# Performance work log

Measured on AMD Instinct MI355X. Metric: run time of the kernel, lower is better.

The kernel has to match this reference:

```python
import jax, jax.numpy as jnp
import numpy as np

G, NPG = 2048, 512          # glimpses, points per glimpse
N0 = G * NPG                # 1,048,576 input points
CPG, CPG2 = 128, 32         # clusters per glimpse at level1/level2
M1, M2 = G * CPG, G * CPG2  # 262144, 65536


def _seg_mean_np(x, ids, m):
    cnt = np.bincount(ids, minlength=m).astype(np.float32)
    out = np.stack([np.bincount(ids, weights=x[:, d], minlength=m) for d in range(x.shape[1])], axis=1)
    return (out / np.maximum(cnt, 1.0)[:, None]).astype(np.float32)


def setup_inputs() -> dict:
    key = jax.random.key(0)
    ks = jax.random.split(key, 16)
    rng = np.random.default_rng(0)
    pos_np = (rng.random((N0, 3)) * 4.0).astype(np.float32)
    # voxel_mean_pool level 0: each point -> a cluster within its glimpse
    g_of_pt = np.arange(N0) // NPG
    out_index0 = (g_of_pt * CPG + rng.integers(0, CPG, N0)).astype(np.int64)
    pos1_np = _seg_mean_np(pos_np, out_index0, M1)
    g_of_c1 = np.arange(M1) // CPG
    out_index1 = (g_of_c1 * CPG2 + rng.integers(0, CPG2, M1)).astype(np.int64)
    pos2_np = _seg_mean_np(pos1_np, out_index1, M2)
    out_index2 = (np.arange(M2) // CPG2).astype(np.int64)  # glimpse id per level-2 point

    def w(k, shp, s=0.05):
        return jax.random.normal(k, shp, dtype=jnp.float32) * s

    return {
        "rgb": jax.random.normal(ks[0], (N0, 1), dtype=jnp.float32),
        "pos": jnp.asarray(pos_np), "pos1": jnp.asarray(pos1_np), "pos2": jnp.asarray(pos2_np),
        "out_index0": jnp.asarray(out_index0), "out_index1": jnp.asarray(out_index1),
        "out_index2": jnp.asarray(out_index2),
        "eps": jax.random.normal(ks[1], (G, 128), dtype=jnp.float32),
        # conv1: local (c_in=1 + 3 -> 16), global (16 -> 32)
        "W1l": w(ks[2], (4, 16)), "b1l": jnp.zeros(16), "W1g": w(ks[3], (16, 32)), "b1g": jnp.zeros(32),
        # conv2: (32+3 -> 64), (64 -> 128)
        "W2l": w(ks[4], (35, 64)), "b2l": jnp.zeros(64), "W2g": w(ks[5], (64, 128)), "b2g": jnp.zeros(128),
        # conv3: (128+3 -> 128), (128 -> 256)
        "W3l": w(ks[6], (131, 128)), "b3l": jnp.zeros(128), "W3g": w(ks[7], (128, 256)), "b3g": jnp.zeros(256),
        "Wlin": w(ks[8], (256, 256)), "blin": jnp.zeros(256),
    }


def _point_conv(x_in, pos_in, pos_out, out_index, Wl, bl, Wg, bg):
    # gather relative position of each input point w.r.t. its output center
    rel = pos_in - pos_out[out_index]                      # [E,3]
    h = jax.nn.celu(jnp.concatenate([x_in, rel], -1) @ Wl + bl)  # per-edge MLP
    m = pos_out.shape[0]
    cnt = jax.ops.segment_sum(jnp.ones((h.shape[0],), h.dtype), out_index, num_segments=m)
    agg = jax.ops.segment_sum(h, out_index, num_segments=m) / jnp.maximum(cnt, 1.0)[:, None]
    return agg @ Wg + bg


def reference(rgb, pos, pos1, pos2, out_index0, out_index1, out_index2, eps,
              W1l, b1l, W1g, b1g, W2l, b2l, W2g, b2g, W3l, b3l, W3g, b3g, Wlin, blin):
    f = rgb  # ar=False path: feature = rgb
    f = jax.nn.celu(_point_conv(f, pos, pos1, out_index0, W1l, b1l, W1g, b1g))   # [M1,32]
    f = jax.nn.celu(_point_conv(f, pos1, pos2, out_index1, W2l, b2l, W2g, b2g))  # [M2,128]
    centers = jnp.zeros((G, 3), f.dtype)  # pos_sample = zeros_like(glimpse__center)
    f = jax.nn.celu(_point_conv(f, pos2, centers, out_index2, W3l, b3l, W3g, b3g))  # [G,256]
    out = f @ Wlin + blin
    mu, sg = jnp.split(out, 2, axis=1)
    sigma = jax.nn.softplus(sg)  # to_sigma
    z = mu + sigma * eps         # Normal.rsample
    z_what, z_mask = jnp.split(z, 2, axis=1)
    return z_what, z_mask, mu, sigma, f
```

## Files before the change

### kernel.cpp

```cpp
#include <hip/hip_runtime.h>
#include <hip/hip_bf16.h>
#include <cstddef>

#define G_   2048
#define NPG_ 512
#define CPG_ 128
#define CPG2_ 32

#define OFF_ZW 0
#define OFF_ZM (G_*64)
#define OFF_MU (2*G_*64)
#define OFF_SG (2*G_*64 + G_*128)
#define OFF_F  (2*G_*64 + 2*G_*128)

typedef __attribute__((ext_vector_type(8))) short bf16x8;
typedef __attribute__((ext_vector_type(4))) float f32x4;

__device__ __forceinline__ float celu_f(float x)     { return x > 0.f ? x : __expf(x) - 1.f; }
__device__ __forceinline__ float softplus_f(float x) { return fmaxf(x, 0.f) + __logf(1.f + __expf(-fabsf(x))); }
__device__ __forceinline__ unsigned short f2bf(float x) {
    unsigned u = __float_as_uint(x);
    u += 0x7FFFu + ((u >> 16) & 1u);
    return (unsigned short)(u >> 16);
}
__device__ __forceinline__ unsigned pack2(float a, float b) {
    unsigned ua = __float_as_uint(a); ua += 0x7FFFu + ((ua >> 16) & 1u);
    unsigned ub = __float_as_uint(b); ub += 0x7FFFu + ((ub >> 16) & 1u);
    return (ua >> 16) | (ub & 0xFFFF0000u);
}
__device__ __forceinline__ float bflo(unsigned w) { return __uint_as_float(w << 16); }
__device__ __forceinline__ float bfhi(unsigned w) { return __uint_as_float(w & 0xffff0000u); }
__device__ __forceinline__ bf16x8 ldb8(const unsigned short* p) {
    union { uint2 u[2]; bf16x8 v; } x;
    x.u[0] = *(const uint2*)p;
    x.u[1] = *(const uint2*)(p + 4);
    return x.v;
}

__global__ void k_prep(const float* __restrict__ W2l, const float* __restrict__ W2g,
                       const float* __restrict__ W3l, const float* __restrict__ W3g,
                       const float* __restrict__ Wlin, const float* __restrict__ W1g,
                       unsigned short* __restrict__ w2lT, unsigned short* __restrict__ w2gT,
                       unsigned short* __restrict__ w3lT, unsigned short* __restrict__ w3gT,
                       unsigned short* __restrict__ wlinT, unsigned short* __restrict__ w1gT)
{
    const int tid = blockIdx.x*256 + threadIdx.x, stride = gridDim.x*256;
    for (int i = tid; i < 64*64; i += stride) {
        const int ch = i >> 6, k = i & 63;
        w2lT[i] = f2bf(k < 35 ? W2l[k*64 + ch] : 0.f);
    }
    for (int i = tid; i < 128*64; i += stride) {
        const int ch = i >> 6, k = i & 63;
        w2gT[i] = f2bf(W2g[k*128 + ch]);
    }
    for (int i = tid; i < 128*160; i += stride) {
        const int ch = i / 160, k = i % 160;
        w3lT[i] = f2bf(k < 131 ? W3l[k*128 + ch] : 0.f);
    }
    for (int i = tid; i < 256*128; i += stride) {
        const int ch = i >> 7, k = i & 127;
        w3gT[i] = f2bf(W3g[k*256 + ch]);
    }
    for (int i = tid; i < 256*256; i += stride) {
        const int ch = i >> 8, k = i & 255;
        wlinT[i] = f2bf(Wlin[k*256 + ch]);
    }
    for (int i = tid; i < 32*40; i += stride) {
        const int ch = i / 40, k = i % 40;
        w1gT[i] = f2bf(k < 16 ? W1g[k*32 + ch] : 0.f);
    }
}

__global__ __launch_bounds__(256, 6) void k_fused(
    const float* __restrict__ rgb, const float* __restrict__ pos, const float* __restrict__ pos1,
    const float* __restrict__ pos2, const int* __restrict__ idx0, const int* __restrict__ idx1,
    const float* __restrict__ W1l, const float* __restrict__ b1l,
    const unsigned short* __restrict__ w1gT, const float* __restrict__ b1g,
    const unsigned short* __restrict__ w2lT, const float* __restrict__ b2l,
    const unsigned short* __restrict__ w2gT, const float* __restrict__ b2g,
    const unsigned short* __restrict__ w3lT, const float* __restrict__ b3l,
    unsigned short* __restrict__ aggws)
{
    const int g = blockIdx.x, t = threadIdx.x;
    const int lane = t & 63, wv = t >> 6;
    const int lr = lane & 15, quad = lane >> 4;

    __shared__ __align__(16) unsigned char smem[27008];
    uint2* const spts = (uint2*)smem;
    unsigned short* const aggT = (unsigned short*)(smem + 4096);
    unsigned short* const xs16 = (unsigned short*)smem;
    unsigned short* const HT   = (unsigned short*)smem;
    unsigned short* const xs3  = (unsigned short*)smem;
    int* const cnt   = (int*)(smem + 18432);
    int* const start = (int*)(smem + 18944);
    int* const ctr   = (int*)(smem + 19456);
    int* const cnti  = (int*)(smem + 19968);
    unsigned short* const sT   = (unsigned short*)(smem + 18432);
    unsigned short* const agg2 = (unsigned short*)(smem + 18432);
    float* const red  = (float*)(smem + 18432);
    float* const invc = (float*)(smem + 26880);

    if (t < CPG_) cnt[t] = 0;
    if (t < CPG2_) cnti[t] = 0;
    int slc_r = 0;
    float relx = 0.f, rely = 0.f, relz = 0.f;
    if (t < CPG_) {
        const int c2 = idx1[g*CPG_ + t];
        slc_r = c2 - g*CPG2_;
        relx = pos1[(g*CPG_ + t)*3 + 0] - pos2[c2*3 + 0];
        rely = pos1[(g*CPG_ + t)*3 + 1] - pos2[c2*3 + 1];
        relz = pos1[(g*CPG_ + t)*3 + 2] - pos2[c2*3 + 2];
    }
    for (int i = t; i < 128*8; i += 256) {
        const int r = i >> 3, j = i & 7;
        ((unsigned*)aggT)[r*20 + 8 + j] = 0u;
    }
    __syncthreads();

    float px0[2], prx[2], pry[2], prz[2];
    int plc[2];
    #pragma unroll
    for (int r = 0; r < 2; r++) {
        const int lp = r*256 + t;
        const int p  = g*NPG_ + lp;
        const int c  = idx0[p];
        plc[r] = c - g*CPG_;
        px0[r] = rgb[p];
        prx[r] = pos[p*3+0] - pos1[c*3+0];
        pry[r] = pos[p*3+1] - pos1[c*3+1];
        prz[r] = pos[p*3+2] - pos1[c*3+2];
        atomicAdd(&cnt[plc[r]], 1);
    }
    if (t < CPG_) atomicAdd(&cnti[slc_r], 1);
    __syncthreads();

    if (t < CPG_) {
        int val = cnt[t];
        const int ln = t & 63;
        #pragma unroll
        for (int d = 1; d < 64; d <<= 1) {
            const int v = __shfl_up(val, d, 64);
            if (ln >= d) val += v;
        }
        ctr[t] = val;
    }
    __syncthreads();
    if (t < CPG_) {
        int v = ctr[t];
        if (t >= 64) v += ctr[63];
        const int s = v - cnt[t];
        start[t] = s; ctr[t] = s;
    }
    if (t < CPG2_) invc[t] = 1.f / fmaxf((float)cnti[t], 1.f);
    __syncthreads();

    #pragma unroll
    for (int r = 0; r < 2; r++) {
        const int slot = atomicAdd(&ctr[plc[r]], 1);
        uint2 pk;
        pk.x = pack2(px0[r], prx[r]);
        pk.y = pack2(pry[r], prz[r]);
        spts[slot] = pk;
    }
    __syncthreads();

    {
        const int c = t >> 1, ch0 = (t & 1) * 8;
        float wj[8], wx[8], wy[8], wz[8], bb2[8];
        #pragma unroll
        for (int j = 0; j < 8; j++) {
            wj[j] = W1l[ch0+j]; wx[j] = W1l[16+ch0+j];
            wy[j] = W1l[32+ch0+j]; wz[j] = W1l[48+ch0+j];
            bb2[j] = b1l[ch0+j];
        }
        float a[8];
        #pragma unroll
        for (int j = 0; j < 8; j++) a[j] = 0.f;
        const int n = cnt[c], base = start[c];
        for (int i = 0; i < n; i++) {
            const uint2 pk = spts[base + i];
            const float x0 = bflo(pk.x), rx = bfhi(pk.x);
            const float ry = bflo(pk.y), rz = bfhi(pk.y);
            #pragma unroll
            for (int j = 0; j < 8; j++) {
                const float h = bb2[j] + x0*wj[j] + rx*wx[j] + ry*wy[j] + rz*wz[j];
                a[j] += celu_f(h);
            }
        }
        const float inv = 1.f / fmaxf((float)n, 1.f);
        uint2 q0, q1;
        q0.x = pack2(a[0]*inv, a[1]*inv);
        q0.y = pack2(a[2]*inv, a[3]*inv);
        q1.x = pack2(a[4]*inv, a[5]*inv);
        q1.y = pack2(a[6]*inv, a[7]*inv);
        *(uint2*)&aggT[c*40 + ch0]     = q0;
        *(uint2*)&aggT[c*40 + ch0 + 4] = q1;
    }
    __syncthreads();

    f32x4 c1[2][2];
    {
        #pragma unroll
        for (int nt = 0; nt < 2; nt++) {
            const float bias = b1g[nt*16 + lr];
            c1[nt][0] = (f32x4){bias, bias, bias, bias};
            c1[nt][1] = (f32x4){bias, bias, bias, bias};
        }
        const bf16x8 b0 = *(const bf16x8*)&w1gT[(0*16 + lr)*40 + quad*8];
        const bf16x8 b1 = *(const bf16x8*)&w1gT[(1*16 + lr)*40 + quad*8];
        #pragma unroll
        for (int mt = 0; mt < 2; mt++) {
            const bf16x8 a = *(const bf16x8*)&aggT[((2*wv + mt)*16 + lr)*40 + quad*8];
            c1[0][mt] = __builtin_amdgcn_mfma_f32_16x16x32_bf16(a, b0, c1[0][mt], 0, 0, 0);
            c1[1][mt] = __builtin_amdgcn_mfma_f32_16x16x32_bf16(a, b1, c1[1][mt], 0, 0, 0);
        }
    }
    __syncthreads();

    {
        const uint4 z4 = {0u, 0u, 0u, 0u};
        for (int i = t; i < 528; i += 256) ((uint4*)sT)[i] = z4;
    }
    #pragma unroll
    for (int nt = 0; nt < 2; nt++)
    #pragma unroll
    for (int mt = 0; mt < 2; mt++)
    #pragma unroll
    for (int r = 0; r < 4; r++) {
        const int cl = (2*wv + mt)*16 + quad*4 + r;
        xs16[cl*72 + nt*16 + lr] = f2bf(celu_f(c1[nt][mt][r]));
    }
    if (t < CPG_) {
        xs16[t*72 + 32] = f2bf(relx);
        xs16[t*72 + 33] = f2bf(rely);
        xs16[t*72 + 34] = f2bf(relz);
    }
    for (int i = t; i < 128*29; i += 256) {
        const int r = i / 29, c = 35 + (i - r*29);
        xs16[r*72 + c] = 0;
    }
    __syncthreads();

    if (t < CPG_) sT[slc_r*132 + t] = 0x3F80;
    float hv[8][4];
    {
        const int chn = wv*16 + lr;
        const bf16x8 bw0 = *(const bf16x8*)&w2lT[chn*64 + quad*8];
        const bf16x8 bw1 = *(const bf16x8*)&w2lT[chn*64 + 32 + quad*8];
        const float bias = b2l[chn];
        #pragma unroll
        for (int m = 0; m < 8; m++) {
            f32x4 acc = (f32x4){bias, bias, bias, bias};
            const bf16x8 a0 = *(const bf16x8*)&xs16[(m*16 + lr)*72 + quad*8];
            const bf16x8 a1 = *(const bf16x8*)&xs16[(m*16 + lr)*72 + 32 + quad*8];
            acc = __builtin_amdgcn_mfma_f32_16x16x32_bf16(a0, bw0, acc, 0, 0, 0);
            acc = __builtin_amdgcn_mfma_f32_16x16x32_bf16(a1, bw1, acc, 0, 0, 0);
            #pragma unroll
            for (int r = 0; r < 4; r++) hv[m][r] = celu_f(acc[r]);
        }
    }
    __syncthreads();

    {
        const int chn = wv*16 + lr;
        #pragma unroll
        for (int m = 0; m < 8; m++) {
            uint2 p;
            p.x = pack2(hv[m][0], hv[m][1]);
            p.y = pack2(hv[m][2], hv[m][3]);
            *(uint2*)&HT[chn*136 + m*16 + quad*4] = p;
        }
    }
    __syncthreads();

    float aggv[2][4];
    {
        const int ch = wv*16 + lr;
        f32x4 acc[2];
        acc[0] = (f32x4){0.f, 0.f, 0.f, 0.f};
        acc[1] = (f32x4){0.f, 0.f, 0.f, 0.f};
        #pragma unroll
        for (int ks = 0; ks < 4; ks++) {
            const bf16x8 b = *(const bf16x8*)&HT[ch*136 + ks*32 + quad*8];
            #pragma unroll
            for (int mt = 0; mt < 2; mt++) {
                const bf16x8 a = ldb8(&sT[(mt*16 + lr)*132 + ks*32 + quad*8]);
                acc[mt] = __builtin_amdgcn_mfma_f32_16x16x32_bf16(a, b, acc[mt], 0, 0, 0);
            }
        }
        #pragma unroll
        for (int mt = 0; mt < 2; mt++)
        #pragma unroll
        for (int r = 0; r < 4; r++)
            aggv[mt][r] = acc[mt][r] * invc[mt*16 + quad*4 + r];
    }
    __syncthreads();

    {
        const int ch = wv*16 + lr;
        #pragma unroll
        for (int mt = 0; mt < 2; mt++)
        #pragma unroll
        for (int r = 0; r < 4; r++)
            agg2[(mt*16 + quad*4 + r)*72 + ch] = f2bf(aggv[mt][r]);
    }
    if (t < CPG2_) {
        #pragma unroll
        for (int d = 0; d < 3; d++)
            xs3[t*168 + 128 + d] = f2bf(pos2[(g*CPG2_ + t)*3 + d]);
    }
    for (int i = t; i < 32*29; i += 256) {
        const int r = i / 29, c = 131 + (i - r*29);
        xs3[r*168 + c] = 0;
    }
    __syncthreads();

    {
        f32x4 acc2[2][2];
        int   chn2[2];
        bf16x8 bw[2][2];
        #pragma unroll
        for (int nt = 0; nt < 2; nt++) {
            chn2[nt] = (wv + nt*4)*16 + lr;
            const float bias = b2g[chn2[nt]];
            #pragma unroll
            for (int mt = 0; mt < 2; mt++) acc2[nt][mt] = (f32x4){bias, bias, bias, bias};
            bw[nt][0] = *(const bf16x8*)&w2gT[chn2[nt]*64 + quad*8];
            bw[nt][1] = *(const bf16x8*)&w2gT[chn2[nt]*64 + 32 + quad*8];
        }
        #pragma unroll
        for (int ks = 0; ks < 2; ks++) {
            #pragma unroll
            for (int mt = 0; mt < 2; mt++) {
                const bf16x8 a = *(const bf16x8*)&agg2[(mt*16 + lr)*72 + ks*32 + quad*8];
                acc2[0][mt] = __builtin_amdgcn_mfma_f32_16x16x32_bf16(a, bw[0][ks], acc2[0][mt], 0, 0, 0);
                acc2[1][mt] = __builtin_amdgcn_mfma_f32_16x16x32_bf16(a, bw[1][ks], acc2[1][mt], 0, 0, 0);
            }
        }
        #pragma unroll
        for (int nt = 0; nt < 2; nt++)
        #pragma unroll
        for (int mt = 0; mt < 2; mt++)
        #pragma unroll
        for (int r = 0; r < 4; r++) {
            const int row = mt*16 + quad*4 + r;
            xs3[row*168 + chn2[nt]] = f2bf(celu_f(acc2[nt][mt][r]));
        }
    }
    __syncthreads();

    {
        f32x4 acc[2][2];
        int chn[2];
        #pragma unroll
        for (int nt = 0; nt < 2; nt++) {
            chn[nt] = (wv + nt*4)*16 + lr;
            const float bias = b3l[chn[nt]];
            #pragma unroll
            for (int mt = 0; mt < 2; mt++) acc[nt][mt] = (f32x4){bias, bias, bias, bias};
        }
        #pragma unroll
        for (int ks = 0; ks < 5; ks++) {
            const bf16x8 b0 = *(const bf16x8*)&w3lT[chn[0]*160 + ks*32 + quad*8];
            const bf16x8 b1 = *(const bf16x8*)&w3lT[chn[1]*160 + ks*32 + quad*8];
            #pragma unroll
            for (int mt = 0; mt < 2; mt++) {
                const bf16x8 a = *(const bf16x8*)&xs3[(mt*16 + lr)*168 + ks*32 + quad*8];
                acc[0][mt] = __builtin_amdgcn_mfma_f32_16x16x32_bf16(a, b0, acc[0][mt], 0, 0, 0);
                acc[1][mt] = __builtin_amdgcn_mfma_f32_16x16x32_bf16(a, b1, acc[1][mt], 0, 0, 0);
            }
        }
        #pragma unroll
        for (int nt = 0; nt < 2; nt++)
        #pragma unroll
        for (int mt = 0; mt < 2; mt++) {
            const float p = celu_f(acc[nt][mt][0]) + celu_f(acc[nt][mt][1])
                          + celu_f(acc[nt][mt][2]) + celu_f(acc[nt][mt][3]);
            red[chn[nt]*9 + mt*4 + quad] = p;
        }
    }
    __syncthreads();

    if (t < 128) {
        const float* rp = &red[t*9];
        float a = 0.f;
        #pragma unroll
        for (int p = 0; p < 8; p++) a += rp[p];
        aggws[(size_t)g*128 + t] = f2bf(a * (1.f/32.f));
    }
}

__global__ __launch_bounds__(256) void k_head(
    const unsigned short* __restrict__ aggws,
    const unsigned short* __restrict__ w3gT, const float* __restrict__ b3g,
    const unsigned short* __restrict__ wlinT, const float* __restrict__ blin,
    const float* __restrict__ eps, float* __restrict__ out)
{
    const int g0 = blockIdx.x * 16, t = threadIdx.x;
    const int lane = t & 63, wv = t >> 6;
    const int lr = lane & 15, quad = lane >> 4;
    __shared__ __align__(16) unsigned short aggB[16*136];
    __shared__ __align__(16) unsigned short f3B[16*264];

    {
        const int row = t >> 4, col8 = (t & 15) * 8;
        const uint4 v = ((const uint4*)aggws)[(size_t)g0*16 + t];
        *(uint4*)&aggB[row*136 + col8] = v;
    }
    __syncthreads();

    {
        f32x4 c3[4];
        int ch3[4];
        #pragma unroll
        for (int nt = 0; nt < 4; nt++) {
            ch3[nt] = (wv + nt*4)*16 + lr;
            const float bias = b3g[ch3[nt]];
            c3[nt] = (f32x4){bias, bias, bias, bias};
        }
        #pragma unroll
        for (int ks = 0; ks < 4; ks++) {
            const bf16x8 a = *(const bf16x8*)&aggB[lr*136 + ks*32 + quad*8];
            #pragma unroll
            for (int nt = 0; nt < 4; nt++) {
                const bf16x8 b = *(const bf16x8*)&w3gT[ch3[nt]*128 + ks*32 + quad*8];
                c3[nt] = __builtin_amdgcn_mfma_f32_16x16x32_bf16(a, b, c3[nt], 0, 0, 0);
            }
        }
        #pragma unroll
        for (int nt = 0; nt < 4; nt++)
        #pragma unroll
        for (int r = 0; r < 4; r++) {
            const int row = quad*4 + r;
            const float v = celu_f(c3[nt][r]);
            out[OFF_F + (size_t)(g0 + row)*256 + ch3[nt]] = v;
            f3B[row*264 + ch3[nt]] = f2bf(v);
        }
    }
    __syncthreads();

    {
        f32x4 cl[4];
        int ch4[4];
        #pragma unroll
        for (int nt = 0; nt < 4; nt++) {
            ch4[nt] = (wv + nt*4)*16 + lr;
            const float bias = blin[ch4[nt]];
            cl[nt] = (f32x4){bias, bias, bias, bias};
        }
        #pragma unroll
        for (int ks = 0; ks < 8; ks++) {
            const bf16x8 a = *(const bf16x8*)&f3B[lr*264 + ks*32 + quad*8];
            #pragma unroll
            for (int nt = 0; nt < 4; nt++) {
                const bf16x8 b = *(const bf16x8*)&wlinT[ch4[nt]*256 + ks*32 + quad*8];
                cl[nt] = __builtin_amdgcn_mfma_f32_16x16x32_bf16(a, b, cl[nt], 0, 0, 0);
            }
        }
        #pragma unroll
        for (int nt = 0; nt < 2; nt++)
        #pragma unroll
        for (int r = 0; r < 4; r++) {
            const int row = quad*4 + r;
            const int g = g0 + row;
            const int ch = ch4[nt];
            const float mu    = cl[nt][r];
            const float sigma = softplus_f(cl[nt + 2][r]);
            const float z     = mu + sigma * eps[(size_t)g*128 + ch];
            out[OFF_MU + (size_t)g*128 + ch] = mu;
            out[OFF_SG + (size_t)g*128 + ch] = sigma;
            if (nt == 0) out[OFF_ZW + (size_t)g*64 + ch] = z;
            else         out[OFF_ZM + (size_t)g*64 + (ch - 64)] = z;
        }
    }
}

extern "C" void kernel_launch(void* const* d_in, const int* in_sizes, int n_in,
                              void* d_out, int out_size, void* d_ws, size_t ws_size,
                              hipStream_t stream)
{
    const float* rgb  = (const float*)d_in[0];
    const float* pos  = (const float*)d_in[1];
    const float* pos1 = (const float*)d_in[2];
    const float* pos2 = (const float*)d_in[3];
    const int*   idx0 = (const int*)d_in[4];
    const int*   idx1 = (const int*)d_in[5];
    const float* eps  = (const float*)d_in[7];
    const float* W1l = (const float*)d_in[8],  *b1l = (const float*)d_in[9];
    const float* W1g = (const float*)d_in[10], *b1g = (const float*)d_in[11];
    const float* W2l = (const float*)d_in[12], *b2l = (const float*)d_in[13];
    const float* W2g = (const float*)d_in[14], *b2g = (const float*)d_in[15];
    const float* W3l = (const float*)d_in[16], *b3l = (const float*)d_in[17];
    const float* W3g = (const float*)d_in[18], *b3g = (const float*)d_in[19];
    const float* Wlin = (const float*)d_in[20], *blin = (const float*)d_in[21];

    unsigned short* w2lT  = (unsigned short*)d_ws;
    unsigned short* w2gT  = w2lT + 64*64;
    unsigned short* w3lT  = w2gT + 128*64;
    unsigned short* w3gT  = w3lT + 128*160;
    unsigned short* wlinT = w3gT + 256*128;
    unsigned short* w1gT  = wlinT + 256*256;
    unsigned short* aggws = w1gT + 32*40;
    float* outp = (float*)d_out;

    k_prep <<<64,    256, 0, stream>>>(W2l, W2g, W3l, W3g, Wlin, W1g,
                                       w2lT, w2gT, w3lT, w3gT, wlinT, w1gT);
    k_fused<<<G_,    256, 0, stream>>>(rgb, pos, pos1, pos2, idx0, idx1,
                                       W1l, b1l, w1gT, b1g,
                                       w2lT, b2l, w2gT, b2g, w3lT, b3l, aggws);
    k_head <<<G_/16, 256, 0, stream>>>(aggws, w3gT, b3g, wlinT, blin, eps, outp);
}
```

Measured before the change: 158.3 us.

## Replace level-0 counting sort with direct LDS float atomic accumulation

```diff
diff --git a/kernel.cpp b/kernel.cpp
--- a/kernel.cpp
+++ b/kernel.cpp
@@ -28,8 +28,6 @@
     unsigned ub = __float_as_uint(b); ub += 0x7FFFu + ((ub >> 16) & 1u);
     return (ua >> 16) | (ub & 0xFFFF0000u);
 }
-__device__ __forceinline__ float bflo(unsigned w) { return __uint_as_float(w << 16); }
-__device__ __forceinline__ float bfhi(unsigned w) { return __uint_as_float(w & 0xffff0000u); }
 __device__ __forceinline__ bf16x8 ldb8(const unsigned short* p) {
     union { uint2 u[2]; bf16x8 v; } x;
     x.u[0] = *(const uint2*)p;
@@ -86,22 +84,25 @@
     const int lr = lane & 15, quad = lane >> 4;
 
     __shared__ __align__(16) unsigned char smem[27008];
-    uint2* const spts = (uint2*)smem;
-    unsigned short* const aggT = (unsigned short*)(smem + 4096);
+    float* const aggf = (float*)smem;
+    unsigned short* const aggT = (unsigned short*)(smem + 8192);
     unsigned short* const xs16 = (unsigned short*)smem;
     unsigned short* const HT   = (unsigned short*)smem;
     unsigned short* const xs3  = (unsigned short*)smem;
-    int* const cnt   = (int*)(smem + 18432);
-    int* const start = (int*)(smem + 18944);
-    int* const ctr   = (int*)(smem + 19456);
-    int* const cnti  = (int*)(smem + 19968);
+    float* const cntf  = (float*)(smem + 18432);
+    float* const cntif = (float*)(smem + 18944);
     unsigned short* const sT   = (unsigned short*)(smem + 18432);
     unsigned short* const agg2 = (unsigned short*)(smem + 18432);
     float* const red  = (float*)(smem + 18432);
     float* const invc = (float*)(smem + 26880);
 
-    if (t < CPG_) cnt[t] = 0;
-    if (t < CPG2_) cnti[t] = 0;
+    if (t < CPG_)  cntf[t]  = 0.f;
+    if (t < CPG2_) cntif[t] = 0.f;
+    {
+        const uint4 z4 = {0u, 0u, 0u, 0u};
+        ((uint4*)aggf)[t]       = z4;
+        ((uint4*)aggf)[256 + t] = z4;
+    }
     int slc_r = 0;
     float relx = 0.f, rely = 0.f, relz = 0.f;
     if (t < CPG_) {
@@ -117,85 +118,50 @@
     }
     __syncthreads();
 
-    float px0[2], prx[2], pry[2], prz[2];
-    int plc[2];
-    #pragma unroll
-    for (int r = 0; r < 2; r++) {
-        const int lp = r*256 + t;
-        const int p  = g*NPG_ + lp;
-        const int c  = idx0[p];
-        plc[r] = c - g*CPG_;
-        px0[r] = rgb[p];
-        prx[r] = pos[p*3+0] - pos1[c*3+0];
-        pry[r] = pos[p*3+1] - pos1[c*3+1];
-        prz[r] = pos[p*3+2] - pos1[c*3+2];
-        atomicAdd(&cnt[plc[r]], 1);
-    }
-    if (t < CPG_) atomicAdd(&cnti[slc_r], 1);
-    __syncthreads();
-
-    if (t < CPG_) {
-        int val = cnt[t];
-        const int ln = t & 63;
-        #pragma unroll
-        for (int d = 1; d < 64; d <<= 1) {
-            const int v = __shfl_up(val, d, 64);
-            if (ln >= d) val += v;
-        }
-        ctr[t] = val;
-    }
-    __syncthreads();
-    if (t < CPG_) {
-        int v = ctr[t];
-        if (t >= 64) v += ctr[63];
-        const int s = v - cnt[t];
-        start[t] = s; ctr[t] = s;
-    }
-    if (t < CPG2_) invc[t] = 1.f / fmaxf((float)cnti[t], 1.f);
-    __syncthreads();
-
-    #pragma unroll
-    for (int r = 0; r < 2; r++) {
-        const int slot = atomicAdd(&ctr[plc[r]], 1);
-        uint2 pk;
-        pk.x = pack2(px0[r], prx[r]);
-        pk.y = pack2(pry[r], prz[r]);
-        spts[slot] = pk;
+    {
+        float px0[2], prx[2], pry[2], prz[2];
+        int plc[2];
+        #pragma unroll
+        for (int r = 0; r < 2; r++) {
+            const int lp = r*256 + t;
+            const int p  = g*NPG_ + lp;
+            const int c  = idx0[p];
+            plc[r] = c - g*CPG_;
+            px0[r] = rgb[p];
+            prx[r] = pos[p*3+0] - pos1[c*3+0];
+            pry[r] = pos[p*3+1] - pos1[c*3+1];
+            prz[r] = pos[p*3+2] - pos1[c*3+2];
+        }
+        atomicAdd(&cntf[plc[0]], 1.f);
+        atomicAdd(&cntf[plc[1]], 1.f);
+        if (t < CPG_) atomicAdd(&cntif[slc_r], 1.f);
+        #pragma unroll
+        for (int j = 0; j < 16; j++) {
+            const float wj = W1l[j], wx = W1l[16+j], wy = W1l[32+j], wz = W1l[48+j];
+            const float bb = b1l[j];
+            const float h0 = bb + px0[0]*wj + prx[0]*wx + pry[0]*wy + prz[0]*wz;
+            const float h1 = bb + px0[1]*wj + prx[1]*wx + pry[1]*wy + prz[1]*wz;
+            atomicAdd(&aggf[j*128 + plc[0]], celu_f(h0));
+            atomicAdd(&aggf[j*128 + plc[1]], celu_f(h1));
+        }
     }
     __syncthreads();
 
     {
         const int c = t >> 1, ch0 = (t & 1) * 8;
-        float wj[8], wx[8], wy[8], wz[8], bb2[8];
-        #pragma unroll
-        for (int j = 0; j < 8; j++) {
-            wj[j] = W1l[ch0+j]; wx[j] = W1l[16+ch0+j];
-            wy[j] = W1l[32+ch0+j]; wz[j] = W1l[48+ch0+j];
-            bb2[j] = b1l[ch0+j];
-        }
+        const float inv = 1.f / fmaxf(cntf[c], 1.f);
         float a[8];
         #pragma unroll
-        for (int j = 0; j < 8; j++) a[j] = 0.f;
-        const int n = cnt[c], base = start[c];
-        for (int i = 0; i < n; i++) {
-            const uint2 pk = spts[base + i];
-            const float x0 = bflo(pk.x), rx = bfhi(pk.x);
-            const float ry = bflo(pk.y), rz = bfhi(pk.y);
-            #pragma unroll
-            for (int j = 0; j < 8; j++) {
-                const float h = bb2[j] + x0*wj[j] + rx*wx[j] + ry*wy[j] + rz*wz[j];
-                a[j] += celu_f(h);
-            }
-        }
-        const float inv = 1.f / fmaxf((float)n, 1.f);
+        for (int j = 0; j < 8; j++) a[j] = aggf[(ch0 + j)*128 + c] * inv;
         uint2 q0, q1;
-        q0.x = pack2(a[0]*inv, a[1]*inv);
-        q0.y = pack2(a[2]*inv, a[3]*inv);
-        q1.x = pack2(a[4]*inv, a[5]*inv);
-        q1.y = pack2(a[6]*inv, a[7]*inv);
+        q0.x = pack2(a[0], a[1]);
+        q0.y = pack2(a[2], a[3]);
+        q1.x = pack2(a[4], a[5]);
+        q1.y = pack2(a[6], a[7]);
         *(uint2*)&aggT[c*40 + ch0]     = q0;
         *(uint2*)&aggT[c*40 + ch0 + 4] = q1;
     }
+    if (t < CPG2_) invc[t] = 1.f / fmaxf(cntif[t], 1.f);
     __syncthreads();
 
     f32x4 c1[2][2];
```

New measurement: 229.4 us. 1.45x slower.

## Compute level-0 edge MLP per point before bucketing, accumulate in packed fp16

Applied to the files above, without the earlier changes.

```diff
diff --git a/kernel.cpp b/kernel.cpp
--- a/kernel.cpp
+++ b/kernel.cpp
@@ -15,6 +15,7 @@
 
 typedef __attribute__((ext_vector_type(8))) short bf16x8;
 typedef __attribute__((ext_vector_type(4))) float f32x4;
+typedef _Float16 f16x2 __attribute__((ext_vector_type(2)));
 
 __device__ __forceinline__ float celu_f(float x)     { return x > 0.f ? x : __expf(x) - 1.f; }
 __device__ __forceinline__ float softplus_f(float x) { return fmaxf(x, 0.f) + __logf(1.f + __expf(-fabsf(x))); }
@@ -28,8 +29,6 @@
     unsigned ub = __float_as_uint(b); ub += 0x7FFFu + ((ub >> 16) & 1u);
     return (ua >> 16) | (ub & 0xFFFF0000u);
 }
-__device__ __forceinline__ float bflo(unsigned w) { return __uint_as_float(w << 16); }
-__device__ __forceinline__ float bfhi(unsigned w) { return __uint_as_float(w & 0xffff0000u); }
 __device__ __forceinline__ bf16x8 ldb8(const unsigned short* p) {
     union { uint2 u[2]; bf16x8 v; } x;
     x.u[0] = *(const uint2*)p;
@@ -86,21 +85,21 @@
     const int lr = lane & 15, quad = lane >> 4;
 
     __shared__ __align__(16) unsigned char smem[27008];
-    uint2* const spts = (uint2*)smem;
-    unsigned short* const aggT = (unsigned short*)(smem + 4096);
-    unsigned short* const xs16 = (unsigned short*)smem;
-    unsigned short* const HT   = (unsigned short*)smem;
-    unsigned short* const xs3  = (unsigned short*)smem;
-    int* const cnt   = (int*)(smem + 18432);
-    int* const start = (int*)(smem + 18944);
-    int* const ctr   = (int*)(smem + 19456);
-    int* const cnti  = (int*)(smem + 19968);
+    unsigned short* const spts2 = (unsigned short*)smem;
+    unsigned short* const aggT  = (unsigned short*)(smem + 16384);
+    unsigned short* const xs16  = (unsigned short*)smem;
+    unsigned short* const HT    = (unsigned short*)smem;
+    unsigned short* const xs3   = (unsigned short*)smem;
+    int* const cnt  = (int*)(smem + 25600);
+    int* const ctr  = (int*)(smem + 26112);
+    int* const cnti = (int*)(smem + 26624);
+    int* const wtot = (int*)(smem + 26752);
     unsigned short* const sT   = (unsigned short*)(smem + 18432);
     unsigned short* const agg2 = (unsigned short*)(smem + 18432);
     float* const red  = (float*)(smem + 18432);
     float* const invc = (float*)(smem + 26880);
 
-    if (t < CPG_) cnt[t] = 0;
+    if (t < CPG_)  cnt[t]  = 0;
     if (t < CPG2_) cnti[t] = 0;
     int slc_r = 0;
     float relx = 0.f, rely = 0.f, relz = 0.f;
@@ -113,25 +112,45 @@
     }
     for (int i = t; i < 128*8; i += 256) {
         const int r = i >> 3, j = i & 7;
-        ((unsigned*)aggT)[r*20 + 8 + j] = 0u;
-    }
-    __syncthreads();
-
-    float px0[2], prx[2], pry[2], prz[2];
+        ((unsigned*)aggT)[r*18 + 8 + j] = 0u;
+    }
+    const bf16x8 w1g_b0 = *(const bf16x8*)&w1gT[(0*16 + lr)*40 + quad*8];
+    const bf16x8 w1g_b1 = *(const bf16x8*)&w1gT[(1*16 + lr)*40 + quad*8];
+    const float  b1g_0 = b1g[lr], b1g_1 = b1g[16 + lr];
+    __syncthreads();
+
+    unsigned hpk[2][8];
     int plc[2];
-    #pragma unroll
-    for (int r = 0; r < 2; r++) {
-        const int lp = r*256 + t;
-        const int p  = g*NPG_ + lp;
-        const int c  = idx0[p];
-        plc[r] = c - g*CPG_;
-        px0[r] = rgb[p];
-        prx[r] = pos[p*3+0] - pos1[c*3+0];
-        pry[r] = pos[p*3+1] - pos1[c*3+1];
-        prz[r] = pos[p*3+2] - pos1[c*3+2];
-        atomicAdd(&cnt[plc[r]], 1);
-    }
-    if (t < CPG_) atomicAdd(&cnti[slc_r], 1);
+    {
+        float px0[2], prx[2], pry[2], prz[2];
+        #pragma unroll
+        for (int r = 0; r < 2; r++) {
+            const int lp = r*256 + t;
+            const int p  = g*NPG_ + lp;
+            const int c  = idx0[p];
+            plc[r] = c - g*CPG_;
+            px0[r] = rgb[p];
+            prx[r] = pos[p*3+0] - pos1[c*3+0];
+            pry[r] = pos[p*3+1] - pos1[c*3+1];
+            prz[r] = pos[p*3+2] - pos1[c*3+2];
+            atomicAdd(&cnt[plc[r]], 1);
+        }
+        if (t < CPG_) atomicAdd(&cnti[slc_r], 1);
+        #pragma unroll
+        for (int j = 0; j < 16; j += 2) {
+            const float wj0 = W1l[j],   wx0 = W1l[16+j],   wy0 = W1l[32+j],   wz0 = W1l[48+j],   bb0 = b1l[j];
+            const float wj1 = W1l[j+1], wx1 = W1l[16+j+1], wy1 = W1l[32+j+1], wz1 = W1l[48+j+1], bb1 = b1l[j+1];
+            #pragma unroll
+            for (int r = 0; r < 2; r++) {
+                const float h0 = celu_f(bb0 + px0[r]*wj0 + prx[r]*wx0 + pry[r]*wy0 + prz[r]*wz0);
+                const float h1 = celu_f(bb1 + px0[r]*wj1 + prx[r]*wx1 + pry[r]*wy1 + prz[r]*wz1);
+                union { f16x2 h; unsigned u; } pk;
+                pk.h[0] = (_Float16)h0;
+                pk.h[1] = (_Float16)h1;
+                hpk[r][j >> 1] = pk.u;
+            }
+        }
+    }
     __syncthreads();
 
     if (t < CPG_) {
@@ -142,77 +161,78 @@
             const int v = __shfl_up(val, d, 64);
             if (ln >= d) val += v;
         }
-        ctr[t] = val;
-    }
-    __syncthreads();
-    if (t < CPG_) {
-        int v = ctr[t];
-        if (t >= 64) v += ctr[63];
-        const int s = v - cnt[t];
-        start[t] = s; ctr[t] = s;
-    }
+        ctr[t] = val - cnt[t];
+        if (t == 63) *wtot = val;
+    }
+    __syncthreads();
+    if (t >= 64 && t < CPG_) ctr[t] += *wtot;
     if (t < CPG2_) invc[t] = 1.f / fmaxf((float)cnti[t], 1.f);
     __syncthreads();
 
     #pragma unroll
     for (int r = 0; r < 2; r++) {
         const int slot = atomicAdd(&ctr[plc[r]], 1);
-        uint2 pk;
-        pk.x = pack2(px0[r], prx[r]);
-        pk.y = pack2(pry[r], prz[r]);
-        spts[slot] = pk;
-    }
-    __syncthreads();
-
-    {
-        const int c = t >> 1, ch0 = (t & 1) * 8;
-        float wj[8], wx[8], wy[8], wz[8], bb2[8];
+        uint4 q0, q1;
+        q0.x = hpk[r][0]; q0.y = hpk[r][1]; q0.z = hpk[r][2]; q0.w = hpk[r][3];
+        q1.x = hpk[r][4]; q1.y = hpk[r][5]; q1.z = hpk[r][6]; q1.w = hpk[r][7];
+        *(uint4*)&spts2[slot*16]     = q0;
+        *(uint4*)&spts2[slot*16 + 8] = q1;
+    }
+    __syncthreads();
+
+    {
+        const int c = t >> 1, half = t & 1;
+        const int n = cnt[c];
+        const int base = ctr[c] - n;
+        const int n0 = (n + 1) >> 1;
+        const int sI = base + (half ? n0 : 0);
+        const int eI = base + (half ? n  : n0);
+        f16x2 acc[8];
+        #pragma unroll
+        for (int j = 0; j < 8; j++) { union { unsigned u; f16x2 h; } z; z.u = 0u; acc[j] = z.h; }
+        for (int i = sI; i < eI; i++) {
+            const uint4 a = *(const uint4*)&spts2[i*16];
+            const uint4 b = *(const uint4*)&spts2[i*16 + 8];
+            union { unsigned u; f16x2 h; } w;
+            w.u = a.x; acc[0] += w.h;  w.u = a.y; acc[1] += w.h;
+            w.u = a.z; acc[2] += w.h;  w.u = a.w; acc[3] += w.h;
+            w.u = b.x; acc[4] += w.h;  w.u = b.y; acc[5] += w.h;
+            w.u = b.z; acc[6] += w.h;  w.u = b.w; acc[7] += w.h;
+        }
         #pragma unroll
         for (int j = 0; j < 8; j++) {
-            wj[j] = W1l[ch0+j]; wx[j] = W1l[16+ch0+j];
-            wy[j] = W1l[32+ch0+j]; wz[j] = W1l[48+ch0+j];
-            bb2[j] = b1l[ch0+j];
-        }
-        float a[8];
-        #pragma unroll
-        for (int j = 0; j < 8; j++) a[j] = 0.f;
-        const int n = cnt[c], base = start[c];
-        for (int i = 0; i < n; i++) {
-            const uint2 pk = spts[base + i];
-            const float x0 = bflo(pk.x), rx = bfhi(pk.x);
-            const float ry = bflo(pk.y), rz = bfhi(pk.y);
-            #pragma unroll
-            for (int j = 0; j < 8; j++) {
-                const float h = bb2[j] + x0*wj[j] + rx*wx[j] + ry*wy[j] + rz*wz[j];
-                a[j] += celu_f(h);
-            }
+            union { unsigned u; f16x2 h; } s, o;
+            s.h = acc[j];
+            o.u = __shfl_xor(s.u, 1);
+            acc[j] += o.h;
         }
         const float inv = 1.f / fmaxf((float)n, 1.f);
+        const int ch0 = half * 8, j0 = half * 4;
+        float v[8];
+        #pragma unroll
+        for (int k = 0; k < 4; k++) {
+            v[2*k]   = (float)acc[j0+k][0] * inv;
+            v[2*k+1] = (float)acc[j0+k][1] * inv;
+        }
         uint2 q0, q1;
-        q0.x = pack2(a[0]*inv, a[1]*inv);
-        q0.y = pack2(a[2]*inv, a[3]*inv);
-        q1.x = pack2(a[4]*inv, a[5]*inv);
-        q1.y = pack2(a[6]*inv, a[7]*inv);
-        *(uint2*)&aggT[c*40 + ch0]     = q0;
-        *(uint2*)&aggT[c*40 + ch0 + 4] = q1;
+        q0.x = pack2(v[0], v[1]); q0.y = pack2(v[2], v[3]);
+        q1.x = pack2(v[4], v[5]); q1.y = pack2(v[6], v[7]);
+        *(uint2*)&aggT[c*36 + ch0]     = q0;
+        *(uint2*)&aggT[c*36 + ch0 + 4] = q1;
     }
     __syncthreads();
 
     f32x4 c1[2][2];
     {
-        #pragma unroll
-        for (int nt = 0; nt < 2; nt++) {
-            const float bias = b1g[nt*16 + lr];
-            c1[nt][0] = (f32x4){bias, bias, bias, bias};
-            c1[nt][1] = (f32x4){bias, bias, bias, bias};
-        }
-        const bf16x8 b0 = *(const bf16x8*)&w1gT[(0*16 + lr)*40 + quad*8];
-        const bf16x8 b1 = *(const bf16x8*)&w1gT[(1*16 + lr)*40 + quad*8];
+        c1[0][0] = (f32x4){b1g_0, b1g_0, b1g_0, b1g_0};
+        c1[0][1] = c1[0][0];
+        c1[1][0] = (f32x4){b1g_1, b1g_1, b1g_1, b1g_1};
+        c1[1][1] = c1[1][0];
         #pragma unroll
         for (int mt = 0; mt < 2; mt++) {
-            const bf16x8 a = *(const bf16x8*)&aggT[((2*wv + mt)*16 + lr)*40 + quad*8];
-            c1[0][mt] = __builtin_amdgcn_mfma_f32_16x16x32_bf16(a, b0, c1[0][mt], 0, 0, 0);
-            c1[1][mt] = __builtin_amdgcn_mfma_f32_16x16x32_bf16(a, b1, c1[1][mt], 0, 0, 0);
+            const bf16x8 a = ldb8(&aggT[((2*wv + mt)*16 + lr)*36 + quad*8]);
+            c1[0][mt] = __builtin_amdgcn_mfma_f32_16x16x32_bf16(a, w1g_b0, c1[0][mt], 0, 0, 0);
+            c1[1][mt] = __builtin_amdgcn_mfma_f32_16x16x32_bf16(a, w1g_b1, c1[1][mt], 0, 0, 0);
         }
     }
     __syncthreads();
```

After: 168.5 us. 6.4% more time.
